# Kernel tuning notes

Hardware: AMD Instinct MI355X
Metric: run time of the kernel (lower is better)

Reference implementation:

```python
import jax, jax.numpy as jnp
import numpy as np

H, HKV, D, HID = 32, 8, 128, 4096
L, CTX, S = 64, 64, 8192
T = CTX + L
HALF = D // 2
EPS = 1e-6
WP = 4096


def setup_inputs() -> dict:
    key = jax.random.key(0)
    ks = jax.random.split(key, 16)
    f = jnp.float32
    w = 0.02
    return {
        "x": jax.random.normal(ks[0], (1, L, HID), f),
        "x_ctx": jax.random.normal(ks[1], (1, CTX, HID), f),
        "cos_q": jax.random.uniform(ks[2], (1, 1, L, HALF), f, -1.0, 1.0),
        "sin_q": jax.random.uniform(ks[3], (1, 1, L, HALF), f, -1.0, 1.0),
        "cos_k": jax.random.uniform(ks[4], (1, 1, T, HALF), f, -1.0, 1.0),
        "sin_k": jax.random.uniform(ks[5], (1, 1, T, HALF), f, -1.0, 1.0),
        "cache_K_in": jax.random.normal(ks[6], (1, HKV, S, D), f),
        "cache_V_in": jax.random.normal(ks[7], (1, HKV, S, D), f),
        "causal_mask": jnp.ones((1, 1, L, WP + T), dtype=bool),
        "Wq": jax.random.normal(ks[8], (HID, H * D), f) * w,
        "Wk": jax.random.normal(ks[9], (HID, HKV * D), f) * w,
        "Wv": jax.random.normal(ks[10], (HID, HKV * D), f) * w,
        "Wo": jax.random.normal(ks[11], (H * D, HID), f) * w,
        "q_norm_w": jnp.ones((D,), f),
        "k_norm_w": jnp.ones((D,), f),
        "write_pos": WP,
        "rotate": 0,
    }


def _rmsnorm(x, w):
    # normalize over head_dim (last axis)
    var = jnp.mean(x * x, axis=-1, keepdims=True)
    return x * jax.lax.rsqrt(var + EPS) * w


def _rope(x, cos, sin):
    # x: (B, H, T, D); cos/sin: (1, 1, T, HALF) -- rotate-half convention
    x1, x2 = x[..., :HALF], x[..., HALF:]
    return jnp.concatenate([x1 * cos - x2 * sin, x2 * cos + x1 * sin], axis=-1)


def reference(x, x_ctx, cos_q, sin_q, cos_k, sin_k, cache_K_in, cache_V_in,
              causal_mask, Wq, Wk, Wv, Wo, q_norm_w, k_norm_w, write_pos, rotate):
    c = jnp.concatenate([x_ctx, x], axis=1)                  # (1, T, HID)
    q = (x @ Wq).reshape(1, L, H, D)
    k = (c @ Wk).reshape(1, T, HKV, D)
    v = (c @ Wv).reshape(1, T, HKV, D)
    q = _rmsnorm(q, q_norm_w).transpose(0, 2, 1, 3)          # (1, H, L, D)
    k = _rmsnorm(k, k_norm_w).transpose(0, 2, 1, 3)          # (1, HKV, T, D)
    v = v.transpose(0, 2, 1, 3)                               # (1, HKV, T, D)
    q = _rope(q, cos_q, sin_q)
    k = _rope(k, cos_k, sin_k)

    if rotate:  # static Python branch (rotate is a compile-time constant)
        attend_K = jnp.concatenate([cache_K_in[:, :, T:S], k], axis=2)
        attend_V = jnp.concatenate([cache_V_in[:, :, T:S], v], axis=2)
    elif write_pos == 0:
        attend_K, attend_V = k, v
    else:
        attend_K = jnp.concatenate([cache_K_in[:, :, :write_pos], k], axis=2)
        attend_V = jnp.concatenate([cache_V_in[:, :, :write_pos], v], axis=2)

    rep = H // HKV
    scale = jnp.float32(D) ** -0.5
    qg = q.reshape(1, HKV, rep, L, D)
    # grouped attention: broadcast KV heads inline instead of materializing expand
    scores = jnp.einsum('bgrld,bgad->bgrla', qg, attend_K) * scale
    scores = jnp.where(causal_mask[:, :, None], scores, -jnp.inf)  # (1,1,1,L,A) bcast
    probs = jax.nn.softmax(scores, axis=-1)
    o = jnp.einsum('bgrla,bgad->bgrld', probs, attend_V)     # (1, HKV, rep, L, D)
    o = o.reshape(1, H, L, D).transpose(0, 2, 1, 3).reshape(1, L, H * D)
    return (o @ Wo, k, v)
```

## Files before the change

kernel.cpp:

```cpp
#include <hip/hip_runtime.h>

typedef unsigned short u16;
typedef __bf16 bf16x8 __attribute__((ext_vector_type(8)));
typedef float f32x4 __attribute__((ext_vector_type(4)));
typedef u16 u16x8 __attribute__((ext_vector_type(8)));

#define NSPLIT 11
#define ANBLK 6
#define KSPLIT 4
#define OSPLIT 8
#define SCALE_Q 0.08838834764831843f

__device__ __forceinline__ u16 f2bf(float f) {
    unsigned u = __builtin_bit_cast(unsigned, f);
    u += 0x7fff + ((u >> 16) & 1);
    return (u16)(u >> 16);
}
__device__ __forceinline__ float bf2f(u16 h) {
    unsigned u = ((unsigned)h) << 16;
    return __builtin_bit_cast(float, u);
}
__device__ __forceinline__ f32x4 mfma16(bf16x8 a, bf16x8 b, f32x4 c) {
    return __builtin_amdgcn_mfma_f32_16x16x32_bf16(a, b, c, 0, 0, 0);
}
__device__ __forceinline__ void gload16(const float* g, void* lds) {
    __builtin_amdgcn_global_load_lds(
        (const __attribute__((address_space(1))) void*)g,
        (__attribute__((address_space(3))) void*)lds, 16, 0, 0);
}

__global__ __launch_bounds__(256)
void k_prep(const float* __restrict__ x, const float* __restrict__ xctx,
            u16* __restrict__ fragA)
{
    int tid = blockIdx.x * 256 + threadIdx.x;
    int row = tid >> 9;
    int k0 = (tid & 511) << 3;
    const float* src = (row < 64) ? (xctx + (size_t)row * 4096)
                                  : (x + (size_t)(row - 64) * 4096);
    f32x4 v0 = *(const f32x4*)&src[k0];
    f32x4 v1 = *(const f32x4*)&src[k0 + 4];
    u16x8 o;
    o[0] = f2bf(v0[0]); o[1] = f2bf(v0[1]); o[2] = f2bf(v0[2]); o[3] = f2bf(v0[3]);
    o[4] = f2bf(v1[0]); o[5] = f2bf(v1[1]); o[6] = f2bf(v1[2]); o[7] = f2bf(v1[3]);
    int ks32 = k0 >> 5;
    int lg = (k0 >> 3) & 3;
    int rt = row >> 4;
    int l = lg * 16 + (row & 15);
    *(u16x8*)&fragA[(((size_t)ks32 * 8 + rt) * 64 + l) * 8] = o;
}

template<int KS>
__global__ __launch_bounds__(256)
void k_qkv(const u16* __restrict__ fragA,
           const float* __restrict__ Wq, const float* __restrict__ Wk,
           const float* __restrict__ Wv, float* __restrict__ part)
{
    constexpr int KCk = 4096 / KS;
    constexpr int NKT = KCk / 64;
    const int col0 = blockIdx.x * 32;
    const int ksp = blockIdx.y;
    const int ks0 = ksp * KCk;
    const float* W; int ldw, cbase, mat;
    if (col0 < 4096)      { W = Wq; ldw = 4096; cbase = col0;        mat = 0; }
    else if (col0 < 5120) { W = Wk; ldw = 1024; cbase = col0 - 4096; mat = 1; }
    else                  { W = Wv; ldw = 1024; cbase = col0 - 5120; mat = 2; }
    const bool full = (mat != 0);
    const int rowbase = full ? 0 : 64;

    __shared__ __align__(16) float BsF[2][64 * 32];

    const int t = threadIdx.x;
    const int w = t >> 6, l = t & 63;
    const int lm = l & 15, lg = l >> 4;
    const int dk = l >> 3;
    const int dn = (l & 7) << 2;

    bf16x8 af[2][4];
    f32x4 acc[2][2] = {};
    const int rt0 = full ? (w * 2) : (4 + w);

    #define QKV_ISSUE(kt_, buf_)                                               \
    {                                                                          \
        const int kg = ks0 + (kt_) * 64;                                       \
        _Pragma("unroll")                                                      \
        for (int i = 0; i < 2; i++) {                                          \
            int kloc = (w * 2 + i) * 8 + dk;                                   \
            gload16(&W[(size_t)(kg + kloc) * ldw + cbase + dn],                \
                    &BsF[buf_][(w * 2 + i) * 256]);                            \
        }                                                                      \
    }
    #define QKV_ALOAD(p_, kt_)                                                 \
    {                                                                          \
        const int kb32 = (ks0 >> 5) + (kt_) * 2;                               \
        af[p_][0] = *(const bf16x8*)&fragA[(((size_t)kb32 * 8 + rt0) * 64 + l) * 8]; \
        af[p_][1] = *(const bf16x8*)&fragA[(((size_t)(kb32 + 1) * 8 + rt0) * 64 + l) * 8]; \
        if (full) {                                                            \
            af[p_][2] = *(const bf16x8*)&fragA[(((size_t)kb32 * 8 + rt0 + 1) * 64 + l) * 8]; \
            af[p_][3] = *(const bf16x8*)&fragA[(((size_t)(kb32 + 1) * 8 + rt0 + 1) * 64 + l) * 8]; \
        }                                                                      \
    }

    QKV_ISSUE(0, 0);
    QKV_ALOAD(0, 0);
    #pragma unroll
    for (int kt = 0; kt < NKT; kt++) {
        const int cur = kt & 1;
        __syncthreads();
        if (kt + 1 < NKT) {
            QKV_ISSUE(kt + 1, cur ^ 1);
            QKV_ALOAD(cur ^ 1, kt + 1);
        }
        #pragma unroll
        for (int ks = 0; ks < 2; ks++) {
            #pragma unroll
            for (int nt = 0; nt < 2; nt++) {
                bf16x8 bfr;
                #pragma unroll
                for (int e = 0; e < 8; e++)
                    bfr[e] = (__bf16)BsF[cur][(ks * 32 + lg * 8 + e) * 32 + nt * 16 + lm];
                acc[0][nt] = mfma16(af[cur][ks], bfr, acc[0][nt]);
                if (full)
                    acc[1][nt] = mfma16(af[cur][2 + ks], bfr, acc[1][nt]);
            }
        }
    }

    const int wrows = full ? 32 : 16;
    const int mts = full ? 2 : 1;
    #pragma unroll
    for (int mt = 0; mt < 2; mt++) {
        if (mt >= mts) break;
        #pragma unroll
        for (int nt = 0; nt < 2; nt++)
            #pragma unroll
            for (int r = 0; r < 4; r++) {
                int grow = rowbase + w * wrows + mt * 16 + lg * 4 + r;
                part[((size_t)ksp * 128 + grow) * 6144 + col0 + nt * 16 + lm] =
                    acc[mt][nt][r];
            }
    }
    #undef QKV_ISSUE
    #undef QKV_ALOAD
}

template<int KS>
__global__ __launch_bounds__(256)
void k_normrope(const float* __restrict__ part,
                const float* __restrict__ cosq, const float* __restrict__ sinq,
                const float* __restrict__ cosk, const float* __restrict__ sink,
                const float* __restrict__ qnw, const float* __restrict__ knw,
                u16* __restrict__ qb, u16* __restrict__ kb,
                float* __restrict__ outk, float* __restrict__ outv,
                u16* __restrict__ vbw)
{
    int wid = blockIdx.x * 4 + (threadIdx.x >> 6);
    int lane = threadIdx.x & 63;
    if (wid < 2048) {
        int h = wid >> 6, lq = wid & 63;
        size_t ro = (size_t)(64 + lq) * 6144 + h * 128;
        float x1 = 0.f, x2 = 0.f;
        #pragma unroll
        for (int s = 0; s < KS; s++) {
            x1 += part[(size_t)s * 786432 + ro + lane];
            x2 += part[(size_t)s * 786432 + ro + lane + 64];
        }
        float ss = x1 * x1 + x2 * x2;
        #pragma unroll
        for (int off = 32; off; off >>= 1) ss += __shfl_xor(ss, off);
        float rms = rsqrtf(ss * (1.0f / 128.0f) + 1e-6f);
        float a = x1 * rms * qnw[lane];
        float b = x2 * rms * qnw[lane + 64];
        float c = cosq[lq * 64 + lane], s = sinq[lq * 64 + lane];
        u16* qo = qb + ((size_t)h * 64 + lq) * 128;
        qo[lane]      = f2bf((a * c - b * s) * SCALE_Q);
        qo[lane + 64] = f2bf((b * c + a * s) * SCALE_Q);
    } else if (wid < 3072) {
        int rr = wid - 2048;
        int kh = rr >> 7, tt = rr & 127;
        size_t ro = (size_t)tt * 6144 + 4096 + kh * 128;
        float x1 = 0.f, x2 = 0.f;
        #pragma unroll
        for (int s = 0; s < KS; s++) {
            x1 += part[(size_t)s * 786432 + ro + lane];
            x2 += part[(size_t)s * 786432 + ro + lane + 64];
        }
        float ss = x1 * x1 + x2 * x2;
        #pragma unroll
        for (int off = 32; off; off >>= 1) ss += __shfl_xor(ss, off);
        float rms = rsqrtf(ss * (1.0f / 128.0f) + 1e-6f);
        float a = x1 * rms * knw[lane];
        float b = x2 * rms * knw[lane + 64];
        float c = cosk[tt * 64 + lane], s = sink[tt * 64 + lane];
        float o1 = a * c - b * s, o2 = b * c + a * s;
        size_t oi = ((size_t)kh * 128 + tt) * 128;
        outk[oi + lane] = o1; outk[oi + lane + 64] = o2;
        kb[oi + lane] = f2bf(o1); kb[oi + lane + 64] = f2bf(o2);
    } else {
        int rr = wid - 3072;
        int kh = rr >> 7, tt = rr & 127;
        size_t ro = (size_t)tt * 6144 + 5120 + kh * 128;
        float v1 = 0.f, v2 = 0.f;
        #pragma unroll
        for (int s = 0; s < KS; s++) {
            v1 += part[(size_t)s * 786432 + ro + lane];
            v2 += part[(size_t)s * 786432 + ro + lane + 64];
        }
        size_t oi = ((size_t)kh * 128 + tt) * 128;
        outv[oi + lane] = v1; outv[oi + lane + 64] = v2;
        vbw[oi + lane] = f2bf(v1); vbw[oi + lane + 64] = f2bf(v2);
    }
}

__global__ __launch_bounds__(256)
void k_prepkv(const float* __restrict__ cacheK, const float* __restrict__ cacheV,
              const u16* __restrict__ kb, const u16* __restrict__ vb,
              u16* __restrict__ kc, u16* __restrict__ vt)
{
    const int bx = blockIdx.x;
    const int t = threadIdx.x;
    if (bx < 528) {
        __shared__ __align__(16) u16 Ls[64][132];
        int kh = bx / 66, tile = bx % 66;
        int key0 = tile * 64;
        #pragma unroll
        for (int it = 0; it < 8; it++) {
            int fidx = it * 256 + t;
            int row = fidx >> 5;
            int d4 = (fidx & 31) << 2;
            int key = key0 + row;
            ushort4 sv;
            if (key < 4096) {
                float4 v = *(const float4*)&cacheV[((size_t)kh * 8192 + key) * 128 + d4];
                sv.x = f2bf(v.x); sv.y = f2bf(v.y); sv.z = f2bf(v.z); sv.w = f2bf(v.w);
            } else {
                sv = *(const ushort4*)&vb[((size_t)kh * 128 + (key - 4096)) * 128 + d4];
            }
            *(ushort4*)&Ls[row][d4] = sv;
        }
        __syncthreads();
        #pragma unroll
        for (int it = 0; it < 4; it++) {
            int fidx = it * 256 + t;
            int d = fidx >> 3;
            int kc8 = (fidx & 7) << 3;
            u16x8 o;
            #pragma unroll
            for (int j = 0; j < 8; j++) o[j] = Ls[kc8 + j][d];
            *(u16x8*)&vt[((size_t)kh * 128 + d) * 4224 + key0 + kc8] = o;
        }
    } else {
        size_t cidx = (size_t)(bx - 528) * 256 + t;
        int kh = (int)(cidx / 67584);
        int rem = (int)(cidx % 67584);
        int tt = rem >> 4;
        int d8 = (rem & 15) << 3;
        u16x8 o;
        if (tt < 4096) {
            const float* src = &cacheK[((size_t)kh * 8192 + tt) * 128 + d8];
            f32x4 a = *(const f32x4*)src;
            f32x4 b = *(const f32x4*)(src + 4);
            o[0] = f2bf(a[0]); o[1] = f2bf(a[1]); o[2] = f2bf(a[2]); o[3] = f2bf(a[3]);
            o[4] = f2bf(b[0]); o[5] = f2bf(b[1]); o[6] = f2bf(b[2]); o[7] = f2bf(b[3]);
        } else {
            o = *(const u16x8*)&kb[((size_t)kh * 128 + (tt - 4096)) * 128 + d8];
        }
        *(u16x8*)&kc[((size_t)kh * 4224 + tt) * 128 + d8] = o;
    }
}

__global__ __launch_bounds__(256)
void k_attn(const u16* __restrict__ qb, const u16* __restrict__ kcache,
            const u16* __restrict__ vcacheT,
            u16* __restrict__ opart, float* __restrict__ lpart)
{
    const int split = blockIdx.x;
    const int kh = blockIdx.y;
    const int z = blockIdx.z;
    const int t = threadIdx.x;
    const int w = t >> 6, l = t & 63;
    const int lm = l & 15, lg = l >> 4;
    const int rep = z * 2 + (w >> 1);
    const int mh = w & 1;

    __shared__ __align__(16) u16 Ks[64][136];
    __shared__ __align__(16) u16 Vs[128][72];
    __shared__ __align__(16) u16 Ps[4][32][40];

    const u16* qh = qb + ((size_t)(kh * 4 + rep) * 64) * 128;
    bf16x8 aq[2][4];
    #pragma unroll
    for (int mt = 0; mt < 2; mt++)
        #pragma unroll
        for (int ks = 0; ks < 4; ks++)
            aq[mt][ks] = *(const bf16x8*)
                &qh[(size_t)(mh * 32 + mt * 16 + lm) * 128 + ks * 32 + lg * 8];

    const u16* kcb = kcache + (size_t)kh * 4224 * 128;
    const u16* vtb = vcacheT + (size_t)kh * 128 * 4224;

    const int krow = t >> 4;
    const int kdc = (t & 15) << 3;
    const int vd = t >> 3;
    const int vkc = t & 7;

    u16x8 pk[4], pv[4];
    f32x4 accO[2][8] = {};
    float lacc[2][4] = {};

    #define AT_LOAD(key0_)                                                     \
    {                                                                          \
        _Pragma("unroll")                                                      \
        for (int it = 0; it < 4; it++)                                         \
            pk[it] = *(const u16x8*)&kcb[(size_t)((key0_) + it * 16 + krow) * 128 + kdc]; \
        _Pragma("unroll")                                                      \
        for (int it = 0; it < 4; it++)                                         \
            pv[it] = *(const u16x8*)&vtb[(size_t)(it * 32 + vd) * 4224 + (key0_) + vkc * 8]; \
    }
    #define AT_STORE()                                                         \
    {                                                                          \
        _Pragma("unroll")                                                      \
        for (int it = 0; it < 4; it++)                                         \
            *(u16x8*)&Ks[it * 16 + krow][kdc] = pk[it];                        \
        _Pragma("unroll")                                                      \
        for (int it = 0; it < 4; it++) {                                       \
            int d = it * 32 + vd;                                              \
            *(u16x8*)&Vs[d][(vkc ^ ((d >> 2) & 7)) << 3] = pv[it];             \
        }                                                                      \
    }

    AT_LOAD(split * (64 * ANBLK));
    #pragma unroll 1
    for (int kbi = 0; kbi < ANBLK; kbi++) {
        __syncthreads();
        AT_STORE();
        __syncthreads();
        if (kbi + 1 < ANBLK) AT_LOAD(split * (64 * ANBLK) + (kbi + 1) * 64);

        f32x4 sa[2][4] = {};
        #pragma unroll
        for (int ks = 0; ks < 4; ks++) {
            bf16x8 bk[4];
            #pragma unroll
            for (int nt = 0; nt < 4; nt++)
                bk[nt] = *(const bf16x8*)&Ks[nt * 16 + lm][ks * 32 + lg * 8];
            #pragma unroll
            for (int mt = 0; mt < 2; mt++)
                #pragma unroll
                for (int nt = 0; nt < 4; nt++)
                    sa[mt][nt] = mfma16(aq[mt][ks], bk[nt], sa[mt][nt]);
        }

        #pragma unroll
        for (int half = 0; half < 2; half++) {
            #pragma unroll
            for (int mt = 0; mt < 2; mt++)
                #pragma unroll
                for (int nt2 = 0; nt2 < 2; nt2++)
                    #pragma unroll
                    for (int r = 0; r < 4; r++) {
                        float e = __expf(sa[mt][half * 2 + nt2][r]);
                        lacc[mt][r] += e;
                        Ps[w][mt * 16 + lg * 4 + r][nt2 * 16 + lm] = f2bf(e);
                    }
            bf16x8 pa[2];
            #pragma unroll
            for (int mt = 0; mt < 2; mt++)
                pa[mt] = *(const bf16x8*)&Ps[w][mt * 16 + lm][lg * 8];
            #pragma unroll
            for (int dt = 0; dt < 8; dt++) {
                int d = dt * 16 + lm;
                int vswz = ((d >> 2) & 7) << 3;
                bf16x8 vb8 = *(const bf16x8*)&Vs[d][(half * 32 + lg * 8) ^ vswz];
                #pragma unroll
                for (int mt = 0; mt < 2; mt++)
                    accO[mt][dt] = mfma16(pa[mt], vb8, accO[mt][dt]);
            }
        }
    }
    #undef AT_LOAD
    #undef AT_STORE

    #pragma unroll
    for (int mt = 0; mt < 2; mt++)
        #pragma unroll
        for (int r = 0; r < 4; r++) {
            float v = lacc[mt][r];
            v += __shfl_xor(v, 1);
            v += __shfl_xor(v, 2);
            v += __shfl_xor(v, 4);
            v += __shfl_xor(v, 8);
            lacc[mt][r] = v;
        }

    const size_t base = (((size_t)kh * NSPLIT + split) * 4 + rep) * 64 + mh * 32;
    if (lm == 0) {
        #pragma unroll
        for (int mt = 0; mt < 2; mt++)
            #pragma unroll
            for (int r = 0; r < 4; r++)
                lpart[base + mt * 16 + lg * 4 + r] = lacc[mt][r];
    }
    #pragma unroll
    for (int mt = 0; mt < 2; mt++)
        #pragma unroll
        for (int dt = 0; dt < 8; dt++)
            #pragma unroll
            for (int r = 0; r < 4; r++)
                opart[(base + mt * 16 + lg * 4 + r) * 128 + dt * 16 + lm] =
                    f2bf(accO[mt][dt][r]);
}

template<int NSP>
__global__ __launch_bounds__(256)
void k_combine(const u16* __restrict__ opart, const float* __restrict__ lpart,
               u16* __restrict__ obf)
{
    int idx = blockIdx.x * 256 + threadIdx.x;
    int lq = idx >> 9;
    int c8 = (idx & 511) << 3;
    int h = c8 >> 7, d = c8 & 127;
    int kh = h >> 2, rep = h & 3;
    float os[8] = {};
    float ls = 0.f;
    #pragma unroll
    for (int s = 0; s < NSP; s++) {
        size_t b = (((size_t)kh * NSP + s) * 4 + rep) * 64 + lq;
        u16x8 v = *(const u16x8*)&opart[b * 128 + d];
        #pragma unroll
        for (int j = 0; j < 8; j++) os[j] += bf2f(v[j]);
        ls += lpart[b];
    }
    float inv = 1.0f / ls;
    u16x8 o;
    #pragma unroll
    for (int j = 0; j < 8; j++) o[j] = f2bf(os[j] * inv);
    *(u16x8*)&obf[(size_t)lq * 4096 + c8] = o;
}

__global__ __launch_bounds__(256)
void k_oproj(const u16* __restrict__ obf, const float* __restrict__ Wo,
             float* __restrict__ parto)
{
    constexpr int NKT = 4096 / OSPLIT / 64;
    const int col0 = blockIdx.x * 32;
    const int osp = blockIdx.y;
    const int ks0 = osp * (4096 / OSPLIT);

    __shared__ __align__(16) float BsF[2][64 * 32];

    const int t = threadIdx.x;
    const int w = t >> 6, l = t & 63;
    const int lm = l & 15, lg = l >> 4;
    const int dk = l >> 3;
    const int dn = (l & 7) << 2;

    bf16x8 af[2][2];
    f32x4 acc[2] = {};

    #define OP_ISSUE(kt_, buf_)                                                \
    {                                                                          \
        const int kg = ks0 + (kt_) * 64;                                       \
        _Pragma("unroll")                                                      \
        for (int i = 0; i < 2; i++) {                                          \
            int kloc = (w * 2 + i) * 8 + dk;                                   \
            gload16(&Wo[(size_t)(kg + kloc) * 4096 + col0 + dn],               \
                    &BsF[buf_][(w * 2 + i) * 256]);                            \
        }                                                                      \
    }
    #define OP_ALOAD(p_, kt_)                                                  \
    {                                                                          \
        const int kb = ks0 + (kt_) * 64;                                       \
        af[p_][0] = *(const bf16x8*)&obf[(size_t)(w * 16 + lm) * 4096 + kb + lg * 8]; \
        af[p_][1] = *(const bf16x8*)&obf[(size_t)(w * 16 + lm) * 4096 + kb + 32 + lg * 8]; \
    }

    OP_ISSUE(0, 0);
    OP_ALOAD(0, 0);
    #pragma unroll
    for (int kt = 0; kt < NKT; kt++) {
        const int cur = kt & 1;
        __syncthreads();
        if (kt + 1 < NKT) {
            OP_ISSUE(kt + 1, cur ^ 1);
            OP_ALOAD(cur ^ 1, kt + 1);
        }
        #pragma unroll
        for (int ks = 0; ks < 2; ks++) {
            #pragma unroll
            for (int nt = 0; nt < 2; nt++) {
                bf16x8 bfr;
                #pragma unroll
                for (int e = 0; e < 8; e++)
                    bfr[e] = (__bf16)BsF[cur][(ks * 32 + lg * 8 + e) * 32 + nt * 16 + lm];
                acc[nt] = mfma16(af[cur][ks], bfr, acc[nt]);
            }
        }
    }

    #pragma unroll
    for (int nt = 0; nt < 2; nt++)
        #pragma unroll
        for (int r = 0; r < 4; r++)
            parto[((size_t)osp * 64 + w * 16 + lg * 4 + r) * 4096 +
                  col0 + nt * 16 + lm] = acc[nt][r];
    #undef OP_ISSUE
    #undef OP_ALOAD
}

__global__ __launch_bounds__(256)
void k_osum(const float* __restrict__ parto, float* __restrict__ out0)
{
    int idx = blockIdx.x * 256 + threadIdx.x;
    float s = 0.f;
    #pragma unroll
    for (int o = 0; o < OSPLIT; o++)
        s += parto[(size_t)o * 262144 + idx];
    out0[idx] = s;
}

extern "C" void kernel_launch(void* const* d_in, const int* in_sizes, int n_in,
                              void* d_out, int out_size, void* d_ws, size_t ws_size,
                              hipStream_t stream)
{
    (void)in_sizes; (void)n_in; (void)out_size; (void)ws_size;
    const float* x      = (const float*)d_in[0];
    const float* xctx   = (const float*)d_in[1];
    const float* cosq   = (const float*)d_in[2];
    const float* sinq   = (const float*)d_in[3];
    const float* cosk   = (const float*)d_in[4];
    const float* sink   = (const float*)d_in[5];
    const float* cacheK = (const float*)d_in[6];
    const float* cacheV = (const float*)d_in[7];
    const float* Wq     = (const float*)d_in[9];
    const float* Wk     = (const float*)d_in[10];
    const float* Wv     = (const float*)d_in[11];
    const float* Wo     = (const float*)d_in[12];
    const float* qnw    = (const float*)d_in[13];
    const float* knw    = (const float*)d_in[14];

    float* out0 = (float*)d_out;
    float* out1 = out0 + 262144;
    float* out2 = out1 + 131072;

    char* ws = (char*)d_ws;
    float* part  = (float*)(ws + 0);
    u16*   kc    = (u16*)(ws + 0);
    u16*   vt    = (u16*)(ws + 8650752);
    u16*   opart = (u16*)(ws + 17301504);
    float* lpart = (float*)(ws + 23068672);
    float* parto = (float*)(ws + 0);
    u16*   fragA = (u16*)(ws + 25165824);
    u16*   qb    = (u16*)(ws + 25165824);
    u16*   kb    = (u16*)(ws + 25165824 + 524288);
    u16*   vb    = (u16*)(ws + 25165824 + 786432);
    u16*   obf   = (u16*)(ws + 25165824 + 1048576);

    k_prep<<<256, 256, 0, stream>>>(x, xctx, fragA);
    k_qkv<KSPLIT><<<dim3(192, KSPLIT), 256, 0, stream>>>(fragA, Wq, Wk, Wv, part);
    k_normrope<KSPLIT><<<1024, 256, 0, stream>>>(part, cosq, sinq, cosk, sink,
                                                 qnw, knw, qb, kb, out1, out2, vb);
    k_prepkv<<<2640, 256, 0, stream>>>(cacheK, cacheV, kb, vb, kc, vt);
    k_attn<<<dim3(NSPLIT, 8, 2), 256, 0, stream>>>(qb, kc, vt, opart, lpart);
    k_combine<NSPLIT><<<128, 256, 0, stream>>>(opart, lpart, obf);
    k_oproj<<<dim3(128, OSPLIT), 256, 0, stream>>>(obf, Wo, parto);
    k_osum<<<1024, 256, 0, stream>>>(parto, out0);
}
```

Baseline: 80.77 us.

## Restructure QKV GEMM with register-staged bf16 LDS tiles and wider column blocks

The QKV projection kernel now loads weight tiles into registers, converts them to bf16 and stores them to a swizzled LDS layout, instead of using direct global-to-LDS fp32 loads followed by per-element conversion on read. Each block covers 64 output columns with two k-subtiles per pipeline stage and a custom waitcnt+barrier, and the K split rises from 4 to 8 so the grid keeps enough blocks. The aims are vectorized conflict-free B-fragment reads from LDS and fewer barriers. In exchange, register pressure rises and the doubled K split writes twice as many partial sums, which the norm/rope kernel must then reduce.

```diff
diff --git a/kernel.cpp b/kernel.cpp
--- a/kernel.cpp
+++ b/kernel.cpp
@@ -7,7 +7,7 @@
 
 #define NSPLIT 11
 #define ANBLK 6
-#define KSPLIT 4
+#define KSPLIT 8
 #define OSPLIT 8
 #define SCALE_Q 0.08838834764831843f
 
@@ -27,6 +27,13 @@
     __builtin_amdgcn_global_load_lds(
         (const __attribute__((address_space(1))) void*)g,
         (__attribute__((address_space(3))) void*)lds, 16, 0, 0);
+}
+__device__ __forceinline__ void lds_barrier() {
+    __builtin_amdgcn_sched_barrier(0);
+    asm volatile("s_waitcnt lgkmcnt(0)" ::: "memory");
+    __builtin_amdgcn_sched_barrier(0);
+    __builtin_amdgcn_s_barrier();
+    __builtin_amdgcn_sched_barrier(0);
 }
 
 __global__ __launch_bounds__(256)
@@ -58,7 +65,9 @@
 {
     constexpr int KCk = 4096 / KS;
     constexpr int NKT = KCk / 64;
-    const int col0 = blockIdx.x * 32;
+    constexpr int GRP = 2;
+    constexpr int NG = NKT / GRP;
+    const int col0 = blockIdx.x * 64;
     const int ksp = blockIdx.y;
     const int ks0 = ksp * KCk;
     const float* W; int ldw, cbase, mat;
@@ -68,61 +77,82 @@
     const bool full = (mat != 0);
     const int rowbase = full ? 0 : 64;
 
-    __shared__ __align__(16) float BsF[2][64 * 32];
+    __shared__ __align__(16) u16 Bs[2][GRP][64 * 64];
 
     const int t = threadIdx.x;
     const int w = t >> 6, l = t & 63;
     const int lm = l & 15, lg = l >> 4;
-    const int dk = l >> 3;
-    const int dn = (l & 7) << 2;
-
-    bf16x8 af[2][4];
-    f32x4 acc[2][2] = {};
+    const int kp = t >> 3;
+    const int c8 = (t & 7) << 3;
+
+    f32x4 pr[2][GRP][4];
+    f32x4 acc[2][4] = {};
     const int rt0 = full ? (w * 2) : (4 + w);
 
-    #define QKV_ISSUE(kt_, buf_)                                               \
+    #define QKV_LOADG(p_, g_)                                                  \
     {                                                                          \
-        const int kg = ks0 + (kt_) * 64;                                       \
-        _Pragma("unroll")                                                      \
-        for (int i = 0; i < 2; i++) {                                          \
-            int kloc = (w * 2 + i) * 8 + dk;                                   \
-            gload16(&W[(size_t)(kg + kloc) * ldw + cbase + dn],                \
-                    &BsF[buf_][(w * 2 + i) * 256]);                            \
+        _Pragma("unroll")                                                      \
+        for (int s = 0; s < GRP; s++) {                                        \
+            const int kg = ks0 + ((g_) * GRP + s) * 64;                        \
+            const float* r0 = &W[(size_t)(kg + 2 * kp) * ldw + cbase + c8];    \
+            const float* r1 = r0 + ldw;                                        \
+            pr[p_][s][0] = *(const f32x4*)r0;                                  \
+            pr[p_][s][1] = *(const f32x4*)(r0 + 4);                            \
+            pr[p_][s][2] = *(const f32x4*)r1;                                  \
+            pr[p_][s][3] = *(const f32x4*)(r1 + 4);                            \
         }                                                                      \
     }
-    #define QKV_ALOAD(p_, kt_)                                                 \
+    #define QKV_STOREG(buf_, p_)                                               \
     {                                                                          \
-        const int kb32 = (ks0 >> 5) + (kt_) * 2;                               \
-        af[p_][0] = *(const bf16x8*)&fragA[(((size_t)kb32 * 8 + rt0) * 64 + l) * 8]; \
-        af[p_][1] = *(const bf16x8*)&fragA[(((size_t)(kb32 + 1) * 8 + rt0) * 64 + l) * 8]; \
-        if (full) {                                                            \
-            af[p_][2] = *(const bf16x8*)&fragA[(((size_t)kb32 * 8 + rt0 + 1) * 64 + l) * 8]; \
-            af[p_][3] = *(const bf16x8*)&fragA[(((size_t)(kb32 + 1) * 8 + rt0 + 1) * 64 + l) * 8]; \
-        }                                                                      \
-    }
-
-    QKV_ISSUE(0, 0);
-    QKV_ALOAD(0, 0);
-    #pragma unroll
-    for (int kt = 0; kt < NKT; kt++) {
-        const int cur = kt & 1;
-        __syncthreads();
-        if (kt + 1 < NKT) {
-            QKV_ISSUE(kt + 1, cur ^ 1);
-            QKV_ALOAD(cur ^ 1, kt + 1);
-        }
-        #pragma unroll
-        for (int ks = 0; ks < 2; ks++) {
-            #pragma unroll
-            for (int nt = 0; nt < 2; nt++) {
-                bf16x8 bfr;
+        _Pragma("unroll")                                                      \
+        for (int s = 0; s < GRP; s++)                                          \
+            _Pragma("unroll")                                                  \
+            for (int j = 0; j < 8; j++) {                                      \
+                int n = c8 + j;                                                \
+                int jv = j & 3, jh = j >> 2;                                   \
+                ushort2 v2;                                                    \
+                v2.x = f2bf(pr[p_][s][jh][jv]);                                \
+                v2.y = f2bf(pr[p_][s][2 + jh][jv]);                            \
+                int idx = n * 64 + ((2 * kp) ^ (((n >> 1) & 7) << 3));         \
+                *(ushort2*)&Bs[buf_][s][idx] = v2;                             \
+            }                                                                  \
+    }
+
+    QKV_LOADG(0, 0);
+    QKV_STOREG(0, 0);
+    QKV_LOADG(1, 1);
+    lds_barrier();
+
+    #pragma unroll
+    for (int g = 0; g < NG; g++) {
+        const int cur = g & 1;
+        if (g + 2 < NG) QKV_LOADG(cur, g + 2);
+        #pragma unroll
+        for (int s = 0; s < GRP; s++) {
+            const int kt = g * GRP + s;
+            const int kb32 = (ks0 >> 5) + kt * 2;
+            #pragma unroll
+            for (int ks = 0; ks < 2; ks++) {
+                bf16x8 a0 = *(const bf16x8*)
+                    &fragA[(((size_t)(kb32 + ks) * 8 + rt0) * 64 + l) * 8];
+                bf16x8 a1;
+                if (full)
+                    a1 = *(const bf16x8*)
+                        &fragA[(((size_t)(kb32 + ks) * 8 + rt0 + 1) * 64 + l) * 8];
+                const int koff = ks * 32 + lg * 8;
                 #pragma unroll
-                for (int e = 0; e < 8; e++)
-                    bfr[e] = (__bf16)BsF[cur][(ks * 32 + lg * 8 + e) * 32 + nt * 16 + lm];
-                acc[0][nt] = mfma16(af[cur][ks], bfr, acc[0][nt]);
-                if (full)
-                    acc[1][nt] = mfma16(af[cur][2 + ks], bfr, acc[1][nt]);
+                for (int nt = 0; nt < 4; nt++) {
+                    int n = nt * 16 + lm;
+                    bf16x8 b = *(const bf16x8*)
+                        &Bs[cur][s][n * 64 + (koff ^ (((n >> 1) & 7) << 3))];
+                    acc[0][nt] = mfma16(a0, b, acc[0][nt]);
+                    if (full) acc[1][nt] = mfma16(a1, b, acc[1][nt]);
+                }
             }
+        }
+        if (g + 1 < NG) {
+            QKV_STOREG(cur ^ 1, (g + 1) & 1);
+            lds_barrier();
         }
     }
 
@@ -132,7 +162,7 @@
     for (int mt = 0; mt < 2; mt++) {
         if (mt >= mts) break;
         #pragma unroll
-        for (int nt = 0; nt < 2; nt++)
+        for (int nt = 0; nt < 4; nt++)
             #pragma unroll
             for (int r = 0; r < 4; r++) {
                 int grow = rowbase + w * wrows + mt * 16 + lg * 4 + r;
@@ -140,8 +170,8 @@
                     acc[mt][nt][r];
             }
     }
-    #undef QKV_ISSUE
-    #undef QKV_ALOAD
+    #undef QKV_LOADG
+    #undef QKV_STOREG
 }
 
 template<int KS>
@@ -557,7 +587,7 @@
     u16*   obf   = (u16*)(ws + 25165824 + 1048576);
 
     k_prep<<<256, 256, 0, stream>>>(x, xctx, fragA);
-    k_qkv<KSPLIT><<<dim3(192, KSPLIT), 256, 0, stream>>>(fragA, Wq, Wk, Wv, part);
+    k_qkv<KSPLIT><<<dim3(96, KSPLIT), 256, 0, stream>>>(fragA, Wq, Wk, Wv, part);
     k_normrope<KSPLIT><<<1024, 256, 0, stream>>>(part, cosq, sinq, cosk, sink,
                                                  qnw, knw, qb, kb, out1, out2, vb);
     k_prepkv<<<2640, 256, 0, stream>>>(cacheK, cacheV, kb, vb, kc, vt);
```

New measurement: 81.00 us. Within noise of the previous version (+0.3%).
